# Performance work log

Measured on AMD Instinct MI355X. Metric: run time of the kernel, lower is better.

Reference implementation:

```python
import jax, jax.numpy as jnp
import numpy as np
import math
from jax import lax

B, T, GS = 16, 511, 1
OBS, OUT = 60, 30
D, H, L = 1024, 16, 8
DFF, HID = 4096, 100
S = T + GS
DH = D // H
EPS = 1e-5


def _ln(x, g, b):
    m = jnp.mean(x, axis=-1, keepdims=True)
    v = jnp.mean(jnp.square(x - m), axis=-1, keepdims=True)
    return (x - m) * lax.rsqrt(v + EPS) * g + b


def setup_inputs():
    key = jax.random.key(0)
    ks = iter(jax.random.split(key, 32))
    def n(shape):
        return jax.random.normal(next(ks), shape, dtype=jnp.float32) * 0.02
    return {
        "states": jax.random.normal(next(ks), (B, T, OBS), dtype=jnp.float32),
        "goals": jax.random.normal(next(ks), (B, GS, OBS), dtype=jnp.float32),
        "Wtok": n((OBS, D)), "btok": jnp.zeros((D,), jnp.float32),
        "pos": n((1, S, D)),
        "ln1_g": jnp.ones((L, D), jnp.float32), "ln1_b": jnp.zeros((L, D), jnp.float32),
        "Wq": n((L, D, D)), "bq": jnp.zeros((L, D), jnp.float32),
        "Wk": n((L, D, D)), "bk": jnp.zeros((L, D), jnp.float32),
        "Wv": n((L, D, D)), "bv": jnp.zeros((L, D), jnp.float32),
        "Wp": n((L, D, D)), "bp": jnp.zeros((L, D), jnp.float32),
        "ln2_g": jnp.ones((L, D), jnp.float32), "ln2_b": jnp.zeros((L, D), jnp.float32),
        "Wm1": n((L, D, DFF)), "bm1": jnp.zeros((L, DFF), jnp.float32),
        "Wm2": n((L, DFF, D)), "bm2": jnp.zeros((L, D), jnp.float32),
        "lnf_g": jnp.ones((D,), jnp.float32), "lnf_b": jnp.zeros((D,), jnp.float32),
        "Wh1": n((D, HID)), "bh1": jnp.zeros((HID,), jnp.float32),
        "Wh2": n((HID, OUT)), "bh2": jnp.zeros((OUT,), jnp.float32),
    }


def reference(states, goals, Wtok, btok, pos, ln1_g, ln1_b, Wq, bq, Wk, bk, Wv, bv, Wp, bp,
              ln2_g, ln2_b, Wm1, bm1, Wm2, bm2, lnf_g, lnf_b, Wh1, bh1, Wh2, bh2):
    # token + positional embeddings (dropout is identity in eval mode, pdrop=0)
    goal_x = goals @ Wtok + btok + pos[:, :GS]
    state_x = states @ Wtok + btok + pos[:, GS:S]
    x = jnp.concatenate([goal_x, state_x], axis=1)  # (B, S, D)
    mask = jnp.tril(jnp.ones((S, S), dtype=bool))
    scale = 1.0 / math.sqrt(DH)

    def block(x, p):
        g1, b1, wq, bq_, wk, bk_, wv, bv_, wp, bp_, g2, b2, w1, bm1_, w2, bm2_ = p
        h = _ln(x, g1, b1)
        q = (h @ wq + bq_).reshape(B, S, H, DH).transpose(0, 2, 1, 3)  # (B,H,S,DH)
        k = (h @ wk + bk_).reshape(B, S, H, DH).transpose(0, 2, 1, 3)
        v = (h @ wv + bv_).reshape(B, S, H, DH).transpose(0, 2, 1, 3)
        att = jnp.einsum('bhqd,bhkd->bhqk', q, k) * scale
        att = jnp.where(mask, att, -jnp.inf)
        att = jax.nn.softmax(att, axis=-1)
        y = jnp.einsum('bhqk,bhkd->bhqd', att, v)
        y = y.transpose(0, 2, 1, 3).reshape(B, S, D) @ wp + bp_
        x = x + y
        h = _ln(x, g2, b2)
        x = x + (jax.nn.gelu(h @ w1 + bm1_, approximate=False) @ w2 + bm2_)
        return x, None

    x, _ = lax.scan(block, x, (ln1_g, ln1_b, Wq, bq, Wk, bk, Wv, bv, Wp, bp,
                               ln2_g, ln2_b, Wm1, bm1, Wm2, bm2))
    x = _ln(x, lnf_g, lnf_b)[:, GS:]  # drop goal tokens -> (B, T, D)
    h = jax.nn.silu(x @ Wh1 + bh1)
    return h @ Wh2 + bh2
```

## Files before the change

### kernel.cpp

```cpp
#include <hip/hip_runtime.h>
#include <cstdint>
#include <math.h>

#define NB_B   16
#define NB_T   511
#define NB_S   512
#define NB_OBS 60
#define NB_D   1024
#define NB_H   16
#define NB_L   8
#define NB_DFF 4096
#define NB_HID 100
#define NB_OUT 30
#define NB_M   8192

typedef __attribute__((ext_vector_type(8))) short  short8;
typedef __attribute__((ext_vector_type(4))) short  short4v;
typedef __attribute__((ext_vector_type(4))) float  f32x4;
typedef __attribute__((ext_vector_type(8))) __bf16 bf16x8;

template <int N_> struct ic { static constexpr int v = N_; };

__device__ __forceinline__ short f2bf(float f) {
  union { float f; unsigned u; } a; a.f = f;
  unsigned u = a.u + 0x7fffu + ((a.u >> 16) & 1u);
  return (short)(u >> 16);
}

__device__ __forceinline__ void load_lds16(const void* g, void* l) {
  __builtin_amdgcn_global_load_lds(
      (__attribute__((address_space(1))) unsigned int*)(uintptr_t)g,
      (__attribute__((address_space(3))) unsigned int*)(unsigned)(uintptr_t)l,
      16, 0, 0);
}

__device__ __forceinline__ f32x4 mfma16(short8 a, short8 b, f32x4 c) {
  return __builtin_amdgcn_mfma_f32_16x16x32_bf16(
      __builtin_bit_cast(bf16x8, a), __builtin_bit_cast(bf16x8, b), c, 0, 0, 0);
}

__device__ __forceinline__ float gelu_fast(float v) {
  const float t = 1.5957691216057308f * (v + 0.044715f * v * v * v);
  const float e = __expf(fminf(t, 30.f));
  return v * (e / (e + 1.f));
}

__global__ __launch_bounds__(256) void tconv2_kernel(
    const float* __restrict__ src, short* __restrict__ dst,
    int R, int C, size_t sstride, size_t dstride) {
  __shared__ float t[64][65];
  const float* s0 = src + blockIdx.z * sstride;
  short* d0 = dst + blockIdx.z * dstride;
  const int c0 = blockIdx.x * 64, r0 = blockIdx.y * 64;
#pragma unroll
  for (int i = 0; i < 4; i++) {
    const int idx = threadIdx.x + i * 256;
    const int r = idx >> 4, c4 = (idx & 15) * 4;
    const float4 v = *(const float4*)&s0[(size_t)(r0 + r) * C + c0 + c4];
    t[r][c4 + 0] = v.x; t[r][c4 + 1] = v.y; t[r][c4 + 2] = v.z; t[r][c4 + 3] = v.w;
  }
  __syncthreads();
#pragma unroll
  for (int i = 0; i < 2; i++) {
    const int idx = threadIdx.x + i * 256;
    const int c = idx >> 3, g = (idx & 7) * 8;
    short8 o;
#pragma unroll
    for (int j = 0; j < 8; j++) o[j] = f2bf(t[g + j][c]);
    *(short8*)&d0[(size_t)(c0 + c) * R + r0 + g] = o;
  }
}

__global__ __launch_bounds__(256) void whead_prep(
    const float* __restrict__ Wh1, const float* __restrict__ bh1,
    short* __restrict__ Wh1t, float* __restrict__ bh1p) {
  const int idx = blockIdx.x * 256 + threadIdx.x;
  const int n = idx >> 10, k = idx & 1023;
  Wh1t[idx] = (n < NB_HID) ? f2bf(Wh1[k * NB_HID + n]) : (short)0;
  if (idx < 128) bh1p[idx] = (idx < NB_HID) ? bh1[idx] : 0.f;
}

__global__ __launch_bounds__(256) void embed2_kernel(
    const float* __restrict__ states, const float* __restrict__ goals,
    const float* __restrict__ Wtok, const float* __restrict__ btok,
    const float* __restrict__ pos, float* __restrict__ x) {
  const int r0 = blockIdx.x * 8;
  __shared__ float tok[8][NB_OBS];
  for (int idx = threadIdx.x; idx < 8 * NB_OBS; idx += 256) {
    const int r = idx / NB_OBS, o = idx - r * NB_OBS;
    const int row = r0 + r, b = row >> 9, s = row & 511;
    tok[r][o] = (s == 0) ? goals[b * NB_OBS + o]
                         : states[((size_t)b * NB_T + (s - 1)) * NB_OBS + o];
  }
  __syncthreads();
#pragma unroll
  for (int i = 0; i < 4; i++) {
    const int d = threadIdx.x + i * 256;
    float acc[8];
#pragma unroll
    for (int r = 0; r < 8; r++) acc[r] = 0.f;
    for (int o = 0; o < NB_OBS; o++) {
      const float wv = Wtok[o * NB_D + d];
#pragma unroll
      for (int r = 0; r < 8; r++) acc[r] += tok[r][o] * wv;
    }
    const float bt = btok[d];
#pragma unroll
    for (int r = 0; r < 8; r++) {
      const int row = r0 + r, s = row & 511;
      x[(size_t)row * NB_D + d] = acc[r] + bt + pos[(size_t)s * NB_D + d];
    }
  }
}

template <typename OutT>
__global__ __launch_bounds__(256) void ln_kernel(
    const float* __restrict__ xin, const float* __restrict__ gam,
    const float* __restrict__ bet, OutT* __restrict__ outp) {
  const int row = blockIdx.x;
  const int tid = threadIdx.x;
  const float4 v = ((const float4*)(xin + (size_t)row * NB_D))[tid];
  float s = v.x + v.y + v.z + v.w;
  float s2 = v.x * v.x + v.y * v.y + v.z * v.z + v.w * v.w;
#pragma unroll
  for (int o = 32; o; o >>= 1) {
    s += __shfl_down(s, o, 64);
    s2 += __shfl_down(s2, o, 64);
  }
  __shared__ float red[8];
  if ((tid & 63) == 0) { red[tid >> 6] = s; red[4 + (tid >> 6)] = s2; }
  __syncthreads();
  const float S1 = red[0] + red[1] + red[2] + red[3];
  const float S2 = red[4] + red[5] + red[6] + red[7];
  const float mean = S1 * (1.f / NB_D);
  const float var = S2 * (1.f / NB_D) - mean * mean;
  const float rs = rsqrtf(var + 1e-5f);
  const float4 g4 = ((const float4*)gam)[tid];
  const float4 b4 = ((const float4*)bet)[tid];
  const float o0 = (v.x - mean) * rs * g4.x + b4.x;
  const float o1 = (v.y - mean) * rs * g4.y + b4.y;
  const float o2 = (v.z - mean) * rs * g4.z + b4.z;
  const float o3 = (v.w - mean) * rs * g4.w + b4.w;
  if constexpr (sizeof(OutT) == 2) {
    short4v r = {f2bf(o0), f2bf(o1), f2bf(o2), f2bf(o3)};
    *(short4v*)((short*)outp + (size_t)row * NB_D + tid * 4) = r;
  } else {
    ((float4*)((float*)outp + (size_t)row * NB_D))[tid] = make_float4(o0, o1, o2, o3);
  }
}

template <int ACT, bool RESID, typename OutT>
__global__ __launch_bounds__(256) void gemm_bt(
    const short* __restrict__ A, const short* __restrict__ Bt,
    const float* __restrict__ bias, const float* __restrict__ resid,
    OutT* __restrict__ C, int N, int K) {
  __shared__ short As[128][32];
  __shared__ short Bs[128][32];
  const int bm = blockIdx.y * 128, bn = blockIdx.x * 128;
  const int tid = threadIdx.x;
  const int w = tid >> 6, lane = tid & 63;
  const int wr = (w >> 1) * 64, wc = (w & 1) * 64;
  const int rr = lane & 15, sg = lane >> 4;

  f32x4 acc[4][4];
#pragma unroll
  for (int i = 0; i < 4; i++)
#pragma unroll
    for (int j = 0; j < 4; j++) acc[i][j] = f32x4{0.f, 0.f, 0.f, 0.f};

  const int srow0 = w * 32 + (lane >> 2);
  const int sslot = lane & 3;

  for (int k0 = 0; k0 < K; k0 += 32) {
    __syncthreads();
#pragma unroll
    for (int inst = 0; inst < 2; inst++) {
      const int r = srow0 + inst * 16;
      const int sl = sslot ^ ((r >> 1) & 3);
      load_lds16(A + (size_t)(bm + r) * K + k0 + sl * 8, &As[w * 32 + inst * 16][0]);
      load_lds16(Bt + (size_t)(bn + r) * K + k0 + sl * 8, &Bs[w * 32 + inst * 16][0]);
    }
    __syncthreads();
    short8 a[4], b[4];
#pragma unroll
    for (int i = 0; i < 4; i++) {
      const int r = wr + i * 16 + rr;
      a[i] = *(const short8*)&As[r][(sg ^ ((r >> 1) & 3)) * 8];
      const int c = wc + i * 16 + rr;
      b[i] = *(const short8*)&Bs[c][(sg ^ ((c >> 1) & 3)) * 8];
    }
#pragma unroll
    for (int i = 0; i < 4; i++)
#pragma unroll
      for (int j = 0; j < 4; j++) acc[i][j] = mfma16(a[i], b[j], acc[i][j]);
  }

#pragma unroll
  for (int j = 0; j < 4; j++) {
    const int col = bn + wc + j * 16 + rr;
    const float bv = bias[col];
#pragma unroll
    for (int i = 0; i < 4; i++) {
#pragma unroll
      for (int q = 0; q < 4; q++) {
        const int row = bm + wr + i * 16 + sg * 4 + q;
        float v = acc[i][j][q] + bv;
        if constexpr (RESID) v += resid[(size_t)row * N + col];
        if constexpr (ACT == 1) v = gelu_fast(v);
        if constexpr (ACT == 2) v = v / (1.f + __expf(-v));
        if constexpr (sizeof(OutT) == 2) C[(size_t)row * N + col] = (OutT)f2bf(v);
        else C[(size_t)row * N + col] = v;
      }
    }
  }
}

template <int N, int K, int ACT, bool RESID, typename OutT>
__device__ __forceinline__ void gemmv3_core(
    const short* __restrict__ A, const short* __restrict__ Bt,
    const float* __restrict__ bias, const float* __restrict__ resid,
    OutT* __restrict__ C) {
  constexpr int NK = K / 32;
  constexpr int NWG = (N / 128) * 32;
  constexpr int Q = NWG / 8;
  __shared__ short As[3][256 * 32];
  __shared__ short Bs[3][128 * 32];

  int wg = blockIdx.x;
  wg = (wg & 7) * Q + (wg >> 3);
  const int bn = (wg >> 5) * 128;
  const int bm = (wg & 31) * 256;

  const int tid = threadIdx.x;
  const int w = tid >> 6, lane = tid & 63;
  const int wm = w >> 1, wn = w & 1;
  const int rr = lane & 15, sg = lane >> 4;
  const int lrow = lane >> 2, lslot = lane & 3;
  const int sslot = lslot ^ ((lrow >> 1) & 3);

  const short* Asrc = A + (size_t)(bm + w * 16 + lrow) * K + sslot * 8;
  const short* Bsrc = Bt + (size_t)(bn + w * 16 + lrow) * K + sslot * 8;
  short* Adst = &As[0][w * 512];
  short* Bdst = &Bs[0][w * 512];

  const int ar = wm * 128 + rr;
  const int br = wn * 64 + rr;
  const int aoff = ar * 32 + ((sg ^ ((ar >> 1) & 3)) * 8);
  const int boff = br * 32 + ((sg ^ ((br >> 1) & 3)) * 8);

  f32x4 acc[8][4];
#pragma unroll
  for (int i = 0; i < 8; i++)
#pragma unroll
    for (int j = 0; j < 4; j++) acc[i][j] = f32x4{0.f, 0.f, 0.f, 0.f};

  auto stage = [&](int sb, int k0) {
    load_lds16(Bsrc + k0,                   Bdst + sb * 4096);
    load_lds16(Bsrc + (size_t)64 * K + k0,  Bdst + sb * 4096 + 2048);
    load_lds16(Asrc + k0,                   Adst + sb * 8192);
    load_lds16(Asrc + (size_t)64 * K + k0,  Adst + sb * 8192 + 2048);
    load_lds16(Asrc + (size_t)128 * K + k0, Adst + sb * 8192 + 4096);
    load_lds16(Asrc + (size_t)192 * K + k0, Adst + sb * 8192 + 6144);
  };

  stage(0, 0);
  stage(1, 32);
  asm volatile("s_waitcnt vmcnt(6)" ::: "memory");
  __builtin_amdgcn_s_barrier();

  auto ktile = [&](auto BUFC, auto SBUFC, int t) {
    constexpr int BUF = decltype(BUFC)::v;
    constexpr int SBUF = decltype(SBUFC)::v;
    const short* Ab = &As[BUF][0];
    const short* Bb = &Bs[BUF][0];
    if (t + 2 < NK) stage(SBUF, (t + 2) * 32);
    short8 a[8], b[4];
#pragma unroll
    for (int i = 0; i < 8; i++) a[i] = *(const short8*)(Ab + aoff + i * 512);
#pragma unroll
    for (int j = 0; j < 4; j++) b[j] = *(const short8*)(Bb + boff + j * 512);
    __builtin_amdgcn_s_setprio(1);
#pragma unroll
    for (int i = 0; i < 8; i++)
#pragma unroll
      for (int j = 0; j < 4; j++) acc[i][j] = mfma16(a[i], b[j], acc[i][j]);
    __builtin_amdgcn_s_setprio(0);
    if (t + 2 < NK)      asm volatile("s_waitcnt vmcnt(6)" ::: "memory");
    else if (t + 1 < NK) asm volatile("s_waitcnt vmcnt(0)" ::: "memory");
    __builtin_amdgcn_s_barrier();
  };

  int t = 0;
#pragma unroll 1
  for (; t + 3 <= NK; t += 3) {
    ktile(ic<0>{}, ic<2>{}, t);
    ktile(ic<1>{}, ic<0>{}, t + 1);
    ktile(ic<2>{}, ic<1>{}, t + 2);
  }
  if constexpr (NK % 3 >= 1) ktile(ic<0>{}, ic<2>{}, NK - NK % 3);
  if constexpr (NK % 3 >= 2) ktile(ic<1>{}, ic<0>{}, NK - NK % 3 + 1);

  const int col0 = bn + wn * 64 + rr;
  float bv[4];
#pragma unroll
  for (int j = 0; j < 4; j++) bv[j] = bias[col0 + j * 16];
#pragma unroll
  for (int i = 0; i < 8; i++) {
#pragma unroll
    for (int q = 0; q < 4; q++) {
      const size_t row = bm + wm * 128 + i * 16 + sg * 4 + q;
      float v0 = acc[i][0][q] + bv[0];
      float v1 = acc[i][1][q] + bv[1];
      float v2 = acc[i][2][q] + bv[2];
      float v3 = acc[i][3][q] + bv[3];
      if constexpr (RESID) {
        const float* rrow = resid + row * N + col0;
        v0 += rrow[0]; v1 += rrow[16]; v2 += rrow[32]; v3 += rrow[48];
      }
      if constexpr (ACT == 1) {
        v0 = gelu_fast(v0); v1 = gelu_fast(v1);
        v2 = gelu_fast(v2); v3 = gelu_fast(v3);
      }
      OutT* crow = C + row * N + col0;
      if constexpr (sizeof(OutT) == 2) {
        crow[0] = (OutT)f2bf(v0); crow[16] = (OutT)f2bf(v1);
        crow[32] = (OutT)f2bf(v2); crow[48] = (OutT)f2bf(v3);
      } else {
        crow[0] = v0; crow[16] = v1; crow[32] = v2; crow[48] = v3;
      }
    }
  }
}

template <int N, int K, int ACT, bool RESID, typename OutT>
__global__ __launch_bounds__(256, 2) void gemmv3(
    const short* __restrict__ A, const short* __restrict__ Bt,
    const float* __restrict__ bias, const float* __restrict__ resid,
    OutT* __restrict__ C) {
  gemmv3_core<N, K, ACT, RESID, OutT>(A, Bt, bias, resid, C);
}

__global__ __launch_bounds__(256, 2) void gemmv3_qkv(
    const short* __restrict__ A, const short* __restrict__ Wt3,
    const float* __restrict__ bq, const float* __restrict__ bk,
    const float* __restrict__ bv, short* __restrict__ outqkv) {
  const int z = blockIdx.z;
  const short* Bt = Wt3 + (size_t)z * NB_D * NB_D;
  const float* bias = (z == 0) ? bq : ((z == 1) ? bk : bv);
  short* C = outqkv + (size_t)z * NB_M * NB_D;
  gemmv3_core<NB_D, NB_D, 0, false, short>(A, Bt, bias, nullptr, C);
}

__global__ __launch_bounds__(256) void attn_kernel(
    const short* __restrict__ qkv, short* __restrict__ out) {
  const int qt = blockIdx.x, hh = blockIdx.y, bb = blockIdx.z;
  const int tid = threadIdx.x;
  const int w = tid >> 6, lane = tid & 63;
  const int rr = lane & 15, sg = lane >> 4;

  const size_t MD = (size_t)NB_M * NB_D;
  const short* Q = qkv;
  const short* K = qkv + MD;
  const short* V = qkv + 2 * MD;

  __shared__ short Ks[64][64];
  __shared__ short Vt[64][64];
  __shared__ short Ps[4][16][64];

  short8 qf[2];
  {
    const size_t qrow = (size_t)bb * NB_S + qt * 64 + w * 16 + rr;
#pragma unroll
    for (int ks = 0; ks < 2; ks++)
      qf[ks] = *(const short8*)&Q[qrow * NB_D + hh * 64 + ks * 32 + sg * 8];
  }

  float mrow[4], lrow[4];
  f32x4 o[4];
#pragma unroll
  for (int j = 0; j < 4; j++) { mrow[j] = -INFINITY; lrow[j] = 0.f; }
#pragma unroll
  for (int nb = 0; nb < 4; nb++) o[nb] = f32x4{0.f, 0.f, 0.f, 0.f};

  for (int kt = 0; kt <= qt; kt++) {
    __syncthreads();
    {
      const int p = lane & 7;
#pragma unroll
      for (int inst = 0; inst < 2; inst++) {
        const int r = w * 16 + inst * 8 + (lane >> 3);
        const int sl = p ^ (r & 7);
        load_lds16(K + ((size_t)bb * NB_S + kt * 64 + r) * NB_D + hh * 64 + sl * 8,
                   &Ks[w * 16 + inst * 8][0]);
      }
    }
    {
#pragma unroll
      for (int cc = 0; cc < 2; cc++) {
        const int c = tid * 2 + cc;
        const int sk = c >> 3, sl = c & 7;
        short8 vv = *(const short8*)&V[((size_t)bb * NB_S + kt * 64 + sk) * NB_D + hh * 64 + sl * 8];
        const int ss = sk >> 3;
#pragma unroll
        for (int j = 0; j < 8; j++) {
          const int dh = sl * 8 + j;
          Vt[dh][(ss ^ (dh & 7)) * 8 + (sk & 7)] = vv[j];
        }
      }
    }
    __syncthreads();

    f32x4 sf[4];
#pragma unroll
    for (int nb = 0; nb < 4; nb++) sf[nb] = f32x4{0.f, 0.f, 0.f, 0.f};
#pragma unroll
    for (int ks = 0; ks < 2; ks++) {
#pragma unroll
      for (int nb = 0; nb < 4; nb++) {
        const int ck = nb * 16 + rr;
        short8 kf = *(const short8*)&Ks[ck][((ks * 4 + sg) ^ (ck & 7)) * 8];
        sf[nb] = mfma16(qf[ks], kf, sf[nb]);
      }
    }
    const int rbase = qt * 64 + w * 16 + sg * 4;
    float pmax[4] = {-INFINITY, -INFINITY, -INFINITY, -INFINITY};
#pragma unroll
    for (int nb = 0; nb < 4; nb++) {
      const int cg = kt * 64 + nb * 16 + rr;
#pragma unroll
      for (int j = 0; j < 4; j++) {
        float sv = sf[nb][j] * 0.125f;
        if (cg > rbase + j) sv = -INFINITY;
        sf[nb][j] = sv;
        pmax[j] = fmaxf(pmax[j], sv);
      }
    }
#pragma unroll
    for (int o1 = 1; o1 < 16; o1 <<= 1)
#pragma unroll
      for (int j = 0; j < 4; j++)
        pmax[j] = fmaxf(pmax[j], __shfl_xor(pmax[j], o1, 64));

    float resc[4], psum[4];
#pragma unroll
    for (int j = 0; j < 4; j++) {
      const float mn = fmaxf(mrow[j], pmax[j]);
      resc[j] = __expf(mrow[j] - mn);
      mrow[j] = mn;
      psum[j] = 0.f;
    }
#pragma unroll
    for (int nb = 0; nb < 4; nb++)
#pragma unroll
      for (int j = 0; j < 4; j++) {
        const float p = __expf(sf[nb][j] - mrow[j]);
        sf[nb][j] = p;
        psum[j] += p;
      }
#pragma unroll
    for (int o1 = 1; o1 < 16; o1 <<= 1)
#pragma unroll
      for (int j = 0; j < 4; j++) psum[j] += __shfl_xor(psum[j], o1, 64);
#pragma unroll
    for (int j = 0; j < 4; j++) lrow[j] = lrow[j] * resc[j] + psum[j];
#pragma unroll
    for (int nb = 0; nb < 4; nb++)
#pragma unroll
      for (int j = 0; j < 4; j++) o[nb][j] *= resc[j];

#pragma unroll
    for (int nb = 0; nb < 4; nb++) {
      const int ck = nb * 16 + rr;
      const int ss = ck >> 3;
#pragma unroll
      for (int j = 0; j < 4; j++) {
        const int rq = sg * 4 + j;
        Ps[w][rq][(ss ^ (rq & 7)) * 8 + (ck & 7)] = f2bf(sf[nb][j]);
      }
    }
#pragma unroll
    for (int ks = 0; ks < 2; ks++) {
      short8 pf = *(const short8*)&Ps[w][rr][((ks * 4 + sg) ^ (rr & 7)) * 8];
#pragma unroll
      for (int nb = 0; nb < 4; nb++) {
        const int dh = nb * 16 + rr;
        short8 vf = *(const short8*)&Vt[dh][((ks * 4 + sg) ^ (dh & 7)) * 8];
        o[nb] = mfma16(pf, vf, o[nb]);
      }
    }
  }

  {
    const size_t orow0 = (size_t)bb * NB_S + qt * 64 + w * 16;
#pragma unroll
    for (int nb = 0; nb < 4; nb++)
#pragma unroll
      for (int j = 0; j < 4; j++) {
        const float v = o[nb][j] / lrow[j];
        out[(orow0 + sg * 4 + j) * NB_D + hh * 64 + nb * 16 + rr] = f2bf(v);
      }
  }
}

__global__ __launch_bounds__(256) void head2_kernel(
    const float* __restrict__ hbuf, const float* __restrict__ Wh2,
    const float* __restrict__ bh2, float* __restrict__ outp) {
  __shared__ float hs[8][NB_HID];
  const int g0 = blockIdx.x * 8;
  for (int idx = threadIdx.x; idx < 8 * NB_HID; idx += 256) {
    const int r = idx / NB_HID, k = idx - r * NB_HID;
    const int gt = g0 + r;
    const int b = gt / NB_T, tt = gt - b * NB_T;
    hs[r][k] = hbuf[(size_t)(b * NB_S + 1 + tt) * 128 + k];
  }
  __syncthreads();
  const int r = threadIdx.x >> 5, c = threadIdx.x & 31;
  if (c < NB_OUT) {
    float acc = bh2[c];
#pragma unroll
    for (int k = 0; k < NB_HID; k++) acc += hs[r][k] * Wh2[k * NB_OUT + c];
    outp[(size_t)(g0 + r) * NB_OUT + c] = acc;
  }
}

extern "C" void kernel_launch(void* const* d_in, const int* in_sizes, int n_in,
                              void* d_out, int out_size, void* d_ws, size_t ws_size,
                              hipStream_t stream) {
  const float* states = (const float*)d_in[0];
  const float* goals  = (const float*)d_in[1];
  const float* Wtok   = (const float*)d_in[2];
  const float* btok   = (const float*)d_in[3];
  const float* pos    = (const float*)d_in[4];
  const float* ln1_g  = (const float*)d_in[5];
  const float* ln1_b  = (const float*)d_in[6];
  const float* Wq     = (const float*)d_in[7];
  const float* bq     = (const float*)d_in[8];
  const float* Wk     = (const float*)d_in[9];
  const float* bk     = (const float*)d_in[10];
  const float* Wv     = (const float*)d_in[11];
  const float* bv     = (const float*)d_in[12];
  const float* Wp     = (const float*)d_in[13];
  const float* bp     = (const float*)d_in[14];
  const float* ln2_g  = (const float*)d_in[15];
  const float* ln2_b  = (const float*)d_in[16];
  const float* Wm1    = (const float*)d_in[17];
  const float* bm1    = (const float*)d_in[18];
  const float* Wm2    = (const float*)d_in[19];
  const float* bm2    = (const float*)d_in[20];
  const float* lnf_g  = (const float*)d_in[21];
  const float* lnf_b  = (const float*)d_in[22];
  const float* Wh1    = (const float*)d_in[23];
  const float* bh1    = (const float*)d_in[24];
  const float* Wh2    = (const float*)d_in[25];
  const float* bh2    = (const float*)d_in[26];

  char* wsp = (char*)d_ws;
  size_t off = 0;
  auto carve = [&](size_t bytes) -> char* {
    char* p = wsp + off;
    off += (bytes + 1023) & ~(size_t)1023;
    return p;
  };
  short* Wqkv_t = (short*)carve((size_t)NB_L * 3 * NB_D * NB_D * 2);
  short* Wp_t   = (short*)carve((size_t)NB_L * NB_D * NB_D * 2);
  short* Wm1_t  = (short*)carve((size_t)NB_L * NB_DFF * NB_D * 2);
  short* Wm2_t  = (short*)carve((size_t)NB_L * NB_D * NB_DFF * 2);
  float* x      = (float*)carve((size_t)NB_M * NB_D * 4);
  short* h      = (short*)carve((size_t)NB_M * NB_D * 2);
  short* qkvb   = (short*)carve((size_t)3 * NB_M * NB_D * 2);
  short* mlp    = (short*)carve((size_t)NB_M * NB_DFF * 2);
  short* Wh1t   = (short*)carve((size_t)128 * NB_D * 2);
  float* bh1p   = (float*)carve(128 * 4);
  short* attout = mlp;
  float* hbuf   = (float*)qkvb;

  const dim3 thr(256);
  const size_t DD = (size_t)NB_D * NB_D;
  const size_t DF = (size_t)NB_D * NB_DFF;

  tconv2_kernel<<<dim3(16, 16, NB_L), thr, 0, stream>>>(Wq, Wqkv_t + 0 * DD, NB_D, NB_D, DD, 3 * DD);
  tconv2_kernel<<<dim3(16, 16, NB_L), thr, 0, stream>>>(Wk, Wqkv_t + 1 * DD, NB_D, NB_D, DD, 3 * DD);
  tconv2_kernel<<<dim3(16, 16, NB_L), thr, 0, stream>>>(Wv, Wqkv_t + 2 * DD, NB_D, NB_D, DD, 3 * DD);
  tconv2_kernel<<<dim3(16, 16, NB_L), thr, 0, stream>>>(Wp, Wp_t, NB_D, NB_D, DD, DD);
  tconv2_kernel<<<dim3(64, 16, NB_L), thr, 0, stream>>>(Wm1, Wm1_t, NB_D, NB_DFF, DF, DF);
  tconv2_kernel<<<dim3(16, 64, NB_L), thr, 0, stream>>>(Wm2, Wm2_t, NB_DFF, NB_D, DF, DF);
  whead_prep<<<512, thr, 0, stream>>>(Wh1, bh1, Wh1t, bh1p);

  embed2_kernel<<<NB_M / 8, thr, 0, stream>>>(states, goals, Wtok, btok, pos, x);

  for (int l = 0; l < NB_L; l++) {
    ln_kernel<short><<<NB_M, thr, 0, stream>>>(x, ln1_g + l * NB_D, ln1_b + l * NB_D, h);
    gemmv3_qkv<<<dim3(256, 1, 3), thr, 0, stream>>>(
        h, Wqkv_t + (size_t)l * 3 * DD, bq + l * NB_D, bk + l * NB_D, bv + l * NB_D, qkvb);
    attn_kernel<<<dim3(NB_S / 64, NB_H, NB_B), thr, 0, stream>>>(qkvb, attout);
    gemmv3<NB_D, NB_D, 0, true, float><<<256, thr, 0, stream>>>(
        attout, Wp_t + (size_t)l * DD, bp + l * NB_D, x, x);
    ln_kernel<short><<<NB_M, thr, 0, stream>>>(x, ln2_g + l * NB_D, ln2_b + l * NB_D, h);
    gemmv3<NB_DFF, NB_D, 1, false, short><<<1024, thr, 0, stream>>>(
        h, Wm1_t + (size_t)l * DF, bm1 + l * NB_DFF, nullptr, mlp);
    gemmv3<NB_D, NB_DFF, 0, true, float><<<256, thr, 0, stream>>>(
        mlp, Wm2_t + (size_t)l * DF, bm2 + l * NB_D, x, x);
  }

  ln_kernel<short><<<NB_M, thr, 0, stream>>>(x, lnf_g, lnf_b, h);
  gemm_bt<2, false, float><<<dim3(1, NB_M / 128), thr, 0, stream>>>(
      h, Wh1t, bh1p, nullptr, hbuf, 128, NB_D);
  head2_kernel<<<NB_M / 8, thr, 0, stream>>>(hbuf, Wh2, bh2, (float*)d_out);
}
```

Before: 3.494 ms.

## Fuse QKV into one wide GEMM, template tile height, use wave-per-row layernorm

QKV projections now run as a single N=3072 GEMM writing an interleaved row layout, with a precomputed concatenated bias, and attention reads Q/K/V at strided offsets. The GEMM kernel is templated on M tile height so the N=1024 projection and MLP-down GEMMs use 128-row tiles, giving 512 workgroups instead of 256 for better CU fill. LayerNorm is rewritten to process one row per wavefront using xor shuffles, removing the LDS reduction and block barrier. The risks are the smaller tiles lowering data reuse per workgroup and the strided QKV layout affecting attention load efficiency.

```diff
diff --git a/kernel.cpp b/kernel.cpp
--- a/kernel.cpp
+++ b/kernel.cpp
@@ -13,6 +13,7 @@
 #define NB_HID 100
 #define NB_OUT 30
 #define NB_M   8192
+#define QKV_S  3072
 
 typedef __attribute__((ext_vector_type(8))) short  short8;
 typedef __attribute__((ext_vector_type(4))) short  short4v;
@@ -78,6 +79,16 @@
   const int n = idx >> 10, k = idx & 1023;
   Wh1t[idx] = (n < NB_HID) ? f2bf(Wh1[k * NB_HID + n]) : (short)0;
   if (idx < 128) bh1p[idx] = (idx < NB_HID) ? bh1[idx] : 0.f;
+}
+
+__global__ __launch_bounds__(256) void qkvbias_prep(
+    const float* __restrict__ bq, const float* __restrict__ bk,
+    const float* __restrict__ bv, float* __restrict__ outb) {
+  const int idx = blockIdx.x * 256 + threadIdx.x;
+  const int l = idx / QKV_S, r = idx - l * QKV_S;
+  const int z = r >> 10, c = r & 1023;
+  const float* src = (z == 0) ? bq : ((z == 1) ? bk : bv);
+  outb[idx] = src[l * NB_D + c];
 }
 
 __global__ __launch_bounds__(256) void embed2_kernel(
@@ -114,38 +125,43 @@
 }
 
 template <typename OutT>
-__global__ __launch_bounds__(256) void ln_kernel(
+__global__ __launch_bounds__(256) void ln_wave(
     const float* __restrict__ xin, const float* __restrict__ gam,
     const float* __restrict__ bet, OutT* __restrict__ outp) {
-  const int row = blockIdx.x;
-  const int tid = threadIdx.x;
-  const float4 v = ((const float4*)(xin + (size_t)row * NB_D))[tid];
-  float s = v.x + v.y + v.z + v.w;
-  float s2 = v.x * v.x + v.y * v.y + v.z * v.z + v.w * v.w;
+  const int row = blockIdx.x * 4 + (threadIdx.x >> 6);
+  const int lane = threadIdx.x & 63;
+  const float4* src = (const float4*)(xin + (size_t)row * NB_D);
+  float4 v[4];
+  float s = 0.f, s2 = 0.f;
+#pragma unroll
+  for (int i = 0; i < 4; i++) {
+    v[i] = src[lane + 64 * i];
+    s += v[i].x + v[i].y + v[i].z + v[i].w;
+    s2 += v[i].x * v[i].x + v[i].y * v[i].y + v[i].z * v[i].z + v[i].w * v[i].w;
+  }
 #pragma unroll
   for (int o = 32; o; o >>= 1) {
-    s += __shfl_down(s, o, 64);
-    s2 += __shfl_down(s2, o, 64);
-  }
-  __shared__ float red[8];
-  if ((tid & 63) == 0) { red[tid >> 6] = s; red[4 + (tid >> 6)] = s2; }
-  __syncthreads();
-  const float S1 = red[0] + red[1] + red[2] + red[3];
-  const float S2 = red[4] + red[5] + red[6] + red[7];
-  const float mean = S1 * (1.f / NB_D);
-  const float var = S2 * (1.f / NB_D) - mean * mean;
+    s += __shfl_xor(s, o, 64);
+    s2 += __shfl_xor(s2, o, 64);
+  }
+  const float mean = s * (1.f / NB_D);
+  const float var = s2 * (1.f / NB_D) - mean * mean;
   const float rs = rsqrtf(var + 1e-5f);
-  const float4 g4 = ((const float4*)gam)[tid];
-  const float4 b4 = ((const float4*)bet)[tid];
-  const float o0 = (v.x - mean) * rs * g4.x + b4.x;
-  const float o1 = (v.y - mean) * rs * g4.y + b4.y;
-  const float o2 = (v.z - mean) * rs * g4.z + b4.z;
-  const float o3 = (v.w - mean) * rs * g4.w + b4.w;
-  if constexpr (sizeof(OutT) == 2) {
-    short4v r = {f2bf(o0), f2bf(o1), f2bf(o2), f2bf(o3)};
-    *(short4v*)((short*)outp + (size_t)row * NB_D + tid * 4) = r;
-  } else {
-    ((float4*)((float*)outp + (size_t)row * NB_D))[tid] = make_float4(o0, o1, o2, o3);
+#pragma unroll
+  for (int i = 0; i < 4; i++) {
+    const float4 g4 = ((const float4*)gam)[lane + 64 * i];
+    const float4 b4 = ((const float4*)bet)[lane + 64 * i];
+    const float o0 = (v[i].x - mean) * rs * g4.x + b4.x;
+    const float o1 = (v[i].y - mean) * rs * g4.y + b4.y;
+    const float o2 = (v[i].z - mean) * rs * g4.z + b4.z;
+    const float o3 = (v[i].w - mean) * rs * g4.w + b4.w;
+    if constexpr (sizeof(OutT) == 2) {
+      short4v r = {f2bf(o0), f2bf(o1), f2bf(o2), f2bf(o3)};
+      *(short4v*)((short*)outp + (size_t)row * NB_D + (lane + 64 * i) * 4) = r;
+    } else {
+      ((float4*)((float*)outp + (size_t)row * NB_D))[lane + 64 * i] =
+          make_float4(o0, o1, o2, o3);
+    }
   }
 }
 
@@ -215,21 +231,26 @@
   }
 }
 
-template <int N, int K, int ACT, bool RESID, typename OutT>
-__device__ __forceinline__ void gemmv3_core(
+template <int BM, int N, int K, int ACT, bool RESID, typename OutT>
+__device__ __forceinline__ void gemmv4_core(
     const short* __restrict__ A, const short* __restrict__ Bt,
     const float* __restrict__ bias, const float* __restrict__ resid,
     OutT* __restrict__ C) {
+  constexpr int MI = BM / 32;
   constexpr int NK = K / 32;
-  constexpr int NWG = (N / 128) * 32;
-  constexpr int Q = NWG / 8;
-  __shared__ short As[3][256 * 32];
+  constexpr int NBN = N / 128;
+  constexpr int NWG = (NB_M / BM) * NBN;
+  constexpr int QC = NWG / 8;
+  constexpr int L = 2 + BM / 64;
+  constexpr int SA = BM * 32;
+
+  __shared__ short As[3][SA];
   __shared__ short Bs[3][128 * 32];
 
   int wg = blockIdx.x;
-  wg = (wg & 7) * Q + (wg >> 3);
-  const int bn = (wg >> 5) * 128;
-  const int bm = (wg & 31) * 256;
+  wg = (wg & 7) * QC + (wg >> 3);
+  const int bm = (wg / NBN) * BM;
+  const int bn = (wg % NBN) * 128;
 
   const int tid = threadIdx.x;
   const int w = tid >> 6, lane = tid & 63;
@@ -243,29 +264,33 @@
   short* Adst = &As[0][w * 512];
   short* Bdst = &Bs[0][w * 512];
 
-  const int ar = wm * 128 + rr;
+  const int ar = wm * (BM / 2) + rr;
   const int br = wn * 64 + rr;
   const int aoff = ar * 32 + ((sg ^ ((ar >> 1) & 3)) * 8);
   const int boff = br * 32 + ((sg ^ ((br >> 1) & 3)) * 8);
 
-  f32x4 acc[8][4];
-#pragma unroll
-  for (int i = 0; i < 8; i++)
+  f32x4 acc[MI][4];
+#pragma unroll
+  for (int i = 0; i < MI; i++)
 #pragma unroll
     for (int j = 0; j < 4; j++) acc[i][j] = f32x4{0.f, 0.f, 0.f, 0.f};
 
   auto stage = [&](int sb, int k0) {
-    load_lds16(Bsrc + k0,                   Bdst + sb * 4096);
-    load_lds16(Bsrc + (size_t)64 * K + k0,  Bdst + sb * 4096 + 2048);
-    load_lds16(Asrc + k0,                   Adst + sb * 8192);
-    load_lds16(Asrc + (size_t)64 * K + k0,  Adst + sb * 8192 + 2048);
-    load_lds16(Asrc + (size_t)128 * K + k0, Adst + sb * 8192 + 4096);
-    load_lds16(Asrc + (size_t)192 * K + k0, Adst + sb * 8192 + 6144);
+    load_lds16(Bsrc + k0,                  Bdst + sb * 4096);
+    load_lds16(Bsrc + (size_t)64 * K + k0, Bdst + sb * 4096 + 2048);
+#pragma unroll
+    for (int c = 0; c < BM / 64; c++)
+      load_lds16(Asrc + (size_t)(c * 64) * K + k0, Adst + sb * SA + c * 2048);
+  };
+
+  auto gate = [&]() {
+    if constexpr (L == 6) asm volatile("s_waitcnt vmcnt(6)" ::: "memory");
+    else                  asm volatile("s_waitcnt vmcnt(4)" ::: "memory");
   };
 
   stage(0, 0);
   stage(1, 32);
-  asm volatile("s_waitcnt vmcnt(6)" ::: "memory");
+  gate();
   __builtin_amdgcn_s_barrier();
 
   auto ktile = [&](auto BUFC, auto SBUFC, int t) {
@@ -274,18 +299,18 @@
     const short* Ab = &As[BUF][0];
     const short* Bb = &Bs[BUF][0];
     if (t + 2 < NK) stage(SBUF, (t + 2) * 32);
-    short8 a[8], b[4];
-#pragma unroll
-    for (int i = 0; i < 8; i++) a[i] = *(const short8*)(Ab + aoff + i * 512);
+    short8 a[MI], b[4];
+#pragma unroll
+    for (int i = 0; i < MI; i++) a[i] = *(const short8*)(Ab + aoff + i * 512);
 #pragma unroll
     for (int j = 0; j < 4; j++) b[j] = *(const short8*)(Bb + boff + j * 512);
     __builtin_amdgcn_s_setprio(1);
 #pragma unroll
-    for (int i = 0; i < 8; i++)
+    for (int i = 0; i < MI; i++)
 #pragma unroll
       for (int j = 0; j < 4; j++) acc[i][j] = mfma16(a[i], b[j], acc[i][j]);
     __builtin_amdgcn_s_setprio(0);
-    if (t + 2 < NK)      asm volatile("s_waitcnt vmcnt(6)" ::: "memory");
+    if (t + 2 < NK)      gate();
     else if (t + 1 < NK) asm volatile("s_waitcnt vmcnt(0)" ::: "memory");
     __builtin_amdgcn_s_barrier();
   };
@@ -305,10 +330,10 @@
 #pragma unroll
   for (int j = 0; j < 4; j++) bv[j] = bias[col0 + j * 16];
 #pragma unroll
-  for (int i = 0; i < 8; i++) {
+  for (int i = 0; i < MI; i++) {
 #pragma unroll
     for (int q = 0; q < 4; q++) {
-      const size_t row = bm + wm * 128 + i * 16 + sg * 4 + q;
+      const size_t row = bm + wm * (BM / 2) + i * 16 + sg * 4 + q;
       float v0 = acc[i][0][q] + bv[0];
       float v1 = acc[i][1][q] + bv[1];
       float v2 = acc[i][2][q] + bv[2];
@@ -332,23 +357,12 @@
   }
 }
 
-template <int N, int K, int ACT, bool RESID, typename OutT>
-__global__ __launch_bounds__(256, 2) void gemmv3(
+template <int BM, int N, int K, int ACT, bool RESID, typename OutT>
+__global__ __launch_bounds__(256, 2) void gemmv4(
     const short* __restrict__ A, const short* __restrict__ Bt,
     const float* __restrict__ bias, const float* __restrict__ resid,
     OutT* __restrict__ C) {
-  gemmv3_core<N, K, ACT, RESID, OutT>(A, Bt, bias, resid, C);
-}
-
-__global__ __launch_bounds__(256, 2) void gemmv3_qkv(
-    const short* __restrict__ A, const short* __restrict__ Wt3,
-    const float* __restrict__ bq, const float* __restrict__ bk,
-    const float* __restrict__ bv, short* __restrict__ outqkv) {
-  const int z = blockIdx.z;
-  const short* Bt = Wt3 + (size_t)z * NB_D * NB_D;
-  const float* bias = (z == 0) ? bq : ((z == 1) ? bk : bv);
-  short* C = outqkv + (size_t)z * NB_M * NB_D;
-  gemmv3_core<NB_D, NB_D, 0, false, short>(A, Bt, bias, nullptr, C);
+  gemmv4_core<BM, N, K, ACT, RESID, OutT>(A, Bt, bias, resid, C);
 }
 
 __global__ __launch_bounds__(256) void attn_kernel(
@@ -358,11 +372,6 @@
   const int w = tid >> 6, lane = tid & 63;
   const int rr = lane & 15, sg = lane >> 4;
 
-  const size_t MD = (size_t)NB_M * NB_D;
-  const short* Q = qkv;
-  const short* K = qkv + MD;
-  const short* V = qkv + 2 * MD;
-
   __shared__ short Ks[64][64];
   __shared__ short Vt[64][64];
   __shared__ short Ps[4][16][64];
@@ -372,7 +381,7 @@
     const size_t qrow = (size_t)bb * NB_S + qt * 64 + w * 16 + rr;
 #pragma unroll
     for (int ks = 0; ks < 2; ks++)
-      qf[ks] = *(const short8*)&Q[qrow * NB_D + hh * 64 + ks * 32 + sg * 8];
+      qf[ks] = *(const short8*)&qkv[qrow * QKV_S + hh * 64 + ks * 32 + sg * 8];
   }
 
   float mrow[4], lrow[4];
@@ -390,7 +399,7 @@
       for (int inst = 0; inst < 2; inst++) {
         const int r = w * 16 + inst * 8 + (lane >> 3);
         const int sl = p ^ (r & 7);
-        load_lds16(K + ((size_t)bb * NB_S + kt * 64 + r) * NB_D + hh * 64 + sl * 8,
+        load_lds16(qkv + ((size_t)bb * NB_S + kt * 64 + r) * QKV_S + 1024 + hh * 64 + sl * 8,
                    &Ks[w * 16 + inst * 8][0]);
       }
     }
@@ -399,7 +408,7 @@
       for (int cc = 0; cc < 2; cc++) {
         const int c = tid * 2 + cc;
         const int sk = c >> 3, sl = c & 7;
-        short8 vv = *(const short8*)&V[((size_t)bb * NB_S + kt * 64 + sk) * NB_D + hh * 64 + sl * 8];
+        short8 vv = *(const short8*)&qkv[((size_t)bb * NB_S + kt * 64 + sk) * QKV_S + 2048 + hh * 64 + sl * 8];
         const int ss = sk >> 3;
 #pragma unroll
         for (int j = 0; j < 8; j++) {
@@ -567,10 +576,11 @@
   short* Wm2_t  = (short*)carve((size_t)NB_L * NB_D * NB_DFF * 2);
   float* x      = (float*)carve((size_t)NB_M * NB_D * 4);
   short* h      = (short*)carve((size_t)NB_M * NB_D * 2);
-  short* qkvb   = (short*)carve((size_t)3 * NB_M * NB_D * 2);
+  short* qkvb   = (short*)carve((size_t)NB_M * QKV_S * 2);
   short* mlp    = (short*)carve((size_t)NB_M * NB_DFF * 2);
   short* Wh1t   = (short*)carve((size_t)128 * NB_D * 2);
   float* bh1p   = (float*)carve(128 * 4);
+  float* bqkv   = (float*)carve((size_t)NB_L * QKV_S * 4);
   short* attout = mlp;
   float* hbuf   = (float*)qkvb;
 
@@ -585,24 +595,25 @@
   tconv2_kernel<<<dim3(64, 16, NB_L), thr, 0, stream>>>(Wm1, Wm1_t, NB_D, NB_DFF, DF, DF);
   tconv2_kernel<<<dim3(16, 64, NB_L), thr, 0, stream>>>(Wm2, Wm2_t, NB_DFF, NB_D, DF, DF);
   whead_prep<<<512, thr, 0, stream>>>(Wh1, bh1, Wh1t, bh1p);
+  qkvbias_prep<<<96, thr, 0, stream>>>(bq, bk, bv, bqkv);
 
   embed2_kernel<<<NB_M / 8, thr, 0, stream>>>(states, goals, Wtok, btok, pos, x);
 
   for (int l = 0; l < NB_L; l++) {
-    ln_kernel<short><<<NB_M, thr, 0, stream>>>(x, ln1_g + l * NB_D, ln1_b + l * NB_D, h);
-    gemmv3_qkv<<<dim3(256, 1, 3), thr, 0, stream>>>(
-        h, Wqkv_t + (size_t)l * 3 * DD, bq + l * NB_D, bk + l * NB_D, bv + l * NB_D, qkvb);
+    ln_wave<short><<<NB_M / 4, thr, 0, stream>>>(x, ln1_g + l * NB_D, ln1_b + l * NB_D, h);
+    gemmv4<256, QKV_S, NB_D, 0, false, short><<<768, thr, 0, stream>>>(
+        h, Wqkv_t + (size_t)l * 3 * DD, bqkv + (size_t)l * QKV_S, nullptr, qkvb);
     attn_kernel<<<dim3(NB_S / 64, NB_H, NB_B), thr, 0, stream>>>(qkvb, attout);
-    gemmv3<NB_D, NB_D, 0, true, float><<<256, thr, 0, stream>>>(
+    gemmv4<128, NB_D, NB_D, 0, true, float><<<512, thr, 0, stream>>>(
         attout, Wp_t + (size_t)l * DD, bp + l * NB_D, x, x);
-    ln_kernel<short><<<NB_M, thr, 0, stream>>>(x, ln2_g + l * NB_D, ln2_b + l * NB_D, h);
-    gemmv3<NB_DFF, NB_D, 1, false, short><<<1024, thr, 0, stream>>>(
+    ln_wave<short><<<NB_M / 4, thr, 0, stream>>>(x, ln2_g + l * NB_D, ln2_b + l * NB_D, h);
+    gemmv4<256, NB_DFF, NB_D, 1, false, short><<<1024, thr, 0, stream>>>(
         h, Wm1_t + (size_t)l * DF, bm1 + l * NB_DFF, nullptr, mlp);
-    gemmv3<NB_D, NB_DFF, 0, true, float><<<256, thr, 0, stream>>>(
+    gemmv4<128, NB_D, NB_DFF, 0, true, float><<<512, thr, 0, stream>>>(
         mlp, Wm2_t + (size_t)l * DF, bm2 + l * NB_D, x, x);
   }
 
-  ln_kernel<short><<<NB_M, thr, 0, stream>>>(x, lnf_g, lnf_b, h);
+  ln_wave<short><<<NB_M / 4, thr, 0, stream>>>(x, lnf_g, lnf_b, h);
   gemm_bt<2, false, float><<<dim3(1, NB_M / 128), thr, 0, stream>>>(
       h, Wh1t, bh1p, nullptr, hbuf, 128, NB_D);
   head2_kernel<<<NB_M / 8, thr, 0, stream>>>(hbuf, Wh2, bh2, (float*)d_out);
```

After: 2.872 ms. -17.8%, faster.
